# Kernel tuning notes

Measured on AMD Instinct MI355X. Metric: run time of the kernel, lower is better.

Reference implementation:

```python
import jax, jax.numpy as jnp
import numpy as np
import math

B, T, D, NH, HS, NB = 1024, 64, 512, 8, 64, 225  # batch, squares, d_model, heads, head_size, buckets

def _displacement_buckets():
    sq = np.arange(T)
    rank, file = sq // 8, sq % 8
    d_rank = rank[None, :] - rank[:, None]
    d_file = file[None, :] - file[:, None]
    return jnp.asarray((d_rank + 7) * 15 + (d_file + 7))  # (64, 64) in [0, 225)

BUCKET = _displacement_buckets()

def setup_inputs() -> dict:
    key = jax.random.key(0)
    ks = jax.random.split(key, 6)
    return {
        "x": jax.random.normal(ks[0], (B, T, D), dtype=jnp.float32),
        "w_qkv": jax.random.normal(ks[1], (3 * D, D), dtype=jnp.float32) * 0.02,
        "w_proj": jax.random.normal(ks[2], (D, D), dtype=jnp.float32) * 0.02,
        "b_proj": jnp.zeros((D,), dtype=jnp.float32),
        "rel_k": jax.random.normal(ks[3], (NB, HS), dtype=jnp.float32) * 0.02,
        "rel_v": jax.random.normal(ks[4], (NB, HS), dtype=jnp.float32) * 0.02,
    }

def reference(x, w_qkv, w_proj, b_proj, rel_k, rel_v):
    b, t, d = x.shape
    qkv = x @ w_qkv.T                                   # (b, t, 3d)
    qkv = qkv.reshape(b, t, 3, NH, HS)                  # 'b t (three nh h)'
    q, k, v = jnp.moveaxis(qkv, 2, 0).transpose(0, 1, 3, 2, 4)  # each (b, nh, t, h)
    scale = 1.0 / math.sqrt(HS)
    rk = rel_k[BUCKET]                                  # (t, t, h)
    rv = rel_v[BUCKET]                                  # (t, t, h)
    logits = jnp.einsum('bhid,bhjd->bhij', q, k) + jnp.einsum('bhid,ijd->bhij', q, rk)
    attn = jax.nn.softmax(logits * scale, axis=-1)      # (b, nh, t, t)
    out = jnp.einsum('bhij,bhjd->bhid', attn, v) + jnp.einsum('bhij,ijd->bhid', attn, rv)
    out = out.transpose(0, 2, 1, 3).reshape(b, t, d)    # 'b nh t h -> b t (nh h)'
    return out @ w_proj.T + b_proj
```

## Files before the change

kernel.cpp:

```cpp
#include <hip/hip_runtime.h>
#include <hip/hip_bf16.h>
#include <stdint.h>
#include <stddef.h>

typedef __attribute__((ext_vector_type(8))) short bf16x8;
typedef __attribute__((ext_vector_type(4))) float f32x4;

typedef __attribute__((address_space(1))) const unsigned int g_as1;
typedef __attribute__((address_space(3))) unsigned int lds_as3;
__device__ __forceinline__ void gload_lds16(const void* g, void* l) {
  __builtin_amdgcn_global_load_lds((g_as1*)g, (lds_as3*)l, 16, 0, 0);
}

__device__ __forceinline__ unsigned short f2bf(float f) {
  union { float f; unsigned int u; } v; v.f = f;
  unsigned int u = v.u;
  u += 0x7fffu + ((u >> 16) & 1u);
  return (unsigned short)(u >> 16);
}
__device__ __forceinline__ float bf2f(unsigned short s) {
  union { unsigned int u; float f; } v; v.u = ((unsigned int)s) << 16;
  return v.f;
}
__device__ __forceinline__ unsigned cvt_pk_bf16(float lo, float hi) {
  __hip_bfloat162 h2 = __float22bfloat162_rn(make_float2(lo, hi));
  unsigned r;
  __builtin_memcpy(&r, &h2, 4);
  return r;
}


__global__ void prep_kernel(const float* __restrict__ wqkv,
                            const float* __restrict__ wproj,
                            const float* __restrict__ relk,
                            const float* __restrict__ relv,
                            short* __restrict__ wq_t,
                            short* __restrict__ wp_t,
                            short* __restrict__ relk_b,
                            short* __restrict__ relvT_b) {
  const int g = blockIdx.x * 256 + threadIdx.x;
  if (g < 98304) {
    const int row = g >> 6, c8 = g & 63;
    const float* s = wqkv + (size_t)row * 512 + c8 * 8;
    float4 f0 = *(const float4*)s;
    float4 f1 = *(const float4*)(s + 4);
    uint4 w;
    w.x = f2bf(f0.x) | ((unsigned)f2bf(f0.y) << 16);
    w.y = f2bf(f0.z) | ((unsigned)f2bf(f0.w) << 16);
    w.z = f2bf(f1.x) | ((unsigned)f2bf(f1.y) << 16);
    w.w = f2bf(f1.z) | ((unsigned)f2bf(f1.w) << 16);
    const int bn = row >> 7, rl = row & 127, kk = c8 >> 3, c8l = c8 & 7;
    char* d = (char*)wq_t + (size_t)(bn * 8 + kk) * 16384 + rl * 128 +
              ((c8l * 16) ^ ((rl & 7) << 4));
    *(uint4*)d = w;
  } else if (g < 131072) {
    const int g2 = g - 98304;
    const int row = g2 >> 6, c8 = g2 & 63;
    const float* s = wproj + (size_t)row * 512 + c8 * 8;
    float4 f0 = *(const float4*)s;
    float4 f1 = *(const float4*)(s + 4);
    uint4 w;
    w.x = f2bf(f0.x) | ((unsigned)f2bf(f0.y) << 16);
    w.y = f2bf(f0.z) | ((unsigned)f2bf(f0.w) << 16);
    w.z = f2bf(f1.x) | ((unsigned)f2bf(f1.y) << 16);
    w.w = f2bf(f1.z) | ((unsigned)f2bf(f1.w) << 16);
    const int bn = row >> 7, rl = row & 127, kk = c8 >> 3, c8l = c8 & 7;
    char* d = (char*)wp_t + (size_t)(bn * 8 + kk) * 16384 + rl * 128 +
              ((c8l * 16) ^ ((rl & 7) << 4));
    *(uint4*)d = w;
  } else if (g < 133120) {
    const int g3 = g - 131072;
    const int nb = g3 >> 3, c8 = g3 & 7;
    uint4 w = {0u, 0u, 0u, 0u};
    if (nb < 225) {
      const float* s = relk + (size_t)nb * 64 + c8 * 8;
      float4 f0 = *(const float4*)s;
      float4 f1 = *(const float4*)(s + 4);
      w.x = f2bf(f0.x) | ((unsigned)f2bf(f0.y) << 16);
      w.y = f2bf(f0.z) | ((unsigned)f2bf(f0.w) << 16);
      w.z = f2bf(f1.x) | ((unsigned)f2bf(f1.y) << 16);
      w.w = f2bf(f1.z) | ((unsigned)f2bf(f1.w) << 16);
    }
    *(uint4*)(relk_b + nb * 64 + c8 * 8) = w;
  } else {
    const int g4 = g - 133120;
    const int d = g4 >> 5, nb0 = (g4 & 31) * 8;
    unsigned short s[8];
#pragma unroll
    for (int j = 0; j < 8; ++j) {
      const int nb = nb0 + j;
      s[j] = (nb < 225) ? f2bf(relv[(size_t)nb * 64 + d]) : (unsigned short)0;
    }
    uint4 w;
    w.x = s[0] | ((unsigned)s[1] << 16);
    w.y = s[2] | ((unsigned)s[3] << 16);
    w.z = s[4] | ((unsigned)s[5] << 16);
    w.w = s[6] | ((unsigned)s[7] << 16);
    *(uint4*)(relvT_b + d * 256 + nb0) = w;
  }
}

__global__ void xconv_kernel(const float* __restrict__ x, short* __restrict__ x_t) {
  const int g = blockIdx.x * 256 + threadIdx.x;
  const int row = g >> 6, c8 = g & 63;
  const float* s = x + (size_t)row * 512 + c8 * 8;
  float4 f0 = *(const float4*)s;
  float4 f1 = *(const float4*)(s + 4);
  uint4 w;
  w.x = f2bf(f0.x) | ((unsigned)f2bf(f0.y) << 16);
  w.y = f2bf(f0.z) | ((unsigned)f2bf(f0.w) << 16);
  w.z = f2bf(f1.x) | ((unsigned)f2bf(f1.y) << 16);
  w.w = f2bf(f1.z) | ((unsigned)f2bf(f1.w) << 16);
  const int bm = row >> 7, rl = row & 127, kk = c8 >> 3, c8l = c8 & 7;
  char* d = (char*)x_t + (size_t)(bm * 8 + kk) * 16384 + rl * 128 +
            ((c8l * 16) ^ ((rl & 7) << 4));
  *(uint4*)d = w;
}

__global__ __launch_bounds__(256)
void qkv_gemm(const short* __restrict__ x_t, const short* __restrict__ wq_t,
              short* __restrict__ q_g, short* __restrict__ k_g,
              short* __restrict__ vT_g) {
  __shared__ __align__(16) short As[8192];
  __shared__ __align__(16) short Bs[8192];
  const int tid = threadIdx.x;
  const int lane = tid & 63;
  const int l15 = lane & 15, l4 = lane >> 4;
  const int wave = tid >> 6;
  const int wm = wave >> 1, wn = wave & 1;
  const int bid = blockIdx.x;
  const int wg = (bid & 7) * 768 + (bid >> 3);
  const int bn = wg % 12;
  const int bm = wg / 12;
  char* as_ = (char*)As;
  char* bs_ = (char*)Bs;
  const char* abase = (const char*)x_t + (size_t)bm * 131072;
  const char* bbase = (const char*)wq_t + (size_t)bn * 131072;
  const int soff = tid * 16;

  const f32x4 fz = {0.f, 0.f, 0.f, 0.f};
  f32x4 acc[4][4];
#pragma unroll
  for (int mt = 0; mt < 4; ++mt)
#pragma unroll
    for (int nt = 0; nt < 4; ++nt) acc[mt][nt] = fz;

#pragma unroll 1
  for (int kk = 0; kk < 8; ++kk) {
    const char* ga = abase + kk * 16384 + soff;
    const char* gb = bbase + kk * 16384 + soff;
#pragma unroll
    for (int i = 0; i < 4; ++i) {
      gload_lds16(ga + i * 4096, as_ + soff + i * 4096);
      gload_lds16(gb + i * 4096, bs_ + soff + i * 4096);
    }
    __syncthreads();
#pragma unroll
    for (int ki = 0; ki < 2; ++ki) {
      bf16x8 af[4], bfr[4];
#pragma unroll
      for (int mt = 0; mt < 4; ++mt) {
        const int row = 64 * wm + 16 * mt + l15;
        af[mt] = *(const bf16x8*)(as_ + row * 128 + ((64 * ki + 16 * l4) ^ ((row & 7) << 4)));
      }
#pragma unroll
      for (int nt = 0; nt < 4; ++nt) {
        const int row = 64 * wn + 16 * nt + l15;
        bfr[nt] = *(const bf16x8*)(bs_ + row * 128 + ((64 * ki + 16 * l4) ^ ((row & 7) << 4)));
      }
#pragma unroll
      for (int mt = 0; mt < 4; ++mt)
#pragma unroll
        for (int nt = 0; nt < 4; ++nt)
          acc[mt][nt] = __builtin_amdgcn_mfma_f32_16x16x32_bf16(af[mt], bfr[nt], acc[mt][nt], 0, 0, 0);
    }
    __syncthreads();
  }

  const int three = bn >> 2;
  if (three < 2) {
    short* dst = (three == 0) ? q_g : k_g;
#pragma unroll
    for (int mt = 0; mt < 4; ++mt) {
      const int m0 = bm * 128 + 64 * wm + 16 * mt + 4 * l4;
      const int b = m0 >> 6, t0 = m0 & 63;
#pragma unroll
      for (int nt = 0; nt < 4; ++nt) {
        const int n = bn * 128 + 64 * wn + 16 * nt + l15;
        const int h = (n >> 6) & 7, d = n & 63;
        short* p = dst + (size_t)(b * 8 + h) * 4096 + d;
#pragma unroll
        for (int jj = 0; jj < 4; ++jj)
          p[(t0 + jj) * 64] = (short)f2bf(acc[mt][nt][jj]);
      }
    }
  } else {
#pragma unroll
    for (int mt = 0; mt < 4; ++mt) {
      const int m0 = bm * 128 + 64 * wm + 16 * mt + 4 * l4;
      const int b = m0 >> 6, t0 = m0 & 63;
#pragma unroll
      for (int nt = 0; nt < 4; ++nt) {
        const int n = bn * 128 + 64 * wn + 16 * nt + l15;
        const int h = (n >> 6) & 7, d = n & 63;
        uint2 w;
        w.x = cvt_pk_bf16(acc[mt][nt][0], acc[mt][nt][1]);
        w.y = cvt_pk_bf16(acc[mt][nt][2], acc[mt][nt][3]);
        *(uint2*)(vT_g + (size_t)((b * 8 + h) * 64 + d) * 64 + t0) = w;
      }
    }
  }
}

__global__ __launch_bounds__(256, 4)
void attn_kernel(const short* __restrict__ q_g, const short* __restrict__ k_g,
                 const short* __restrict__ vT_g, const short* __restrict__ relk,
                 const short* __restrict__ relvT, short* __restrict__ aout_t) {
  __shared__ __align__(16) short srel_s[64 * 256];
  __shared__ __align__(16) short attn_s[64 * 64];
  const int tid = threadIdx.x, lane = tid & 63, w = tid >> 6;
  const int l15 = lane & 15, l4 = lane >> 4;
  const int bh = blockIdx.x;
  const short* qb = q_g + (size_t)bh * 4096;
  const short* kb = k_g + (size_t)bh * 4096;
  const short* vb = vT_g + (size_t)bh * 4096;
  char* ss = (char*)srel_s;
  char* as = (char*)attn_s;
  const f32x4 fz = {0.f, 0.f, 0.f, 0.f};

  bf16x8 bq[4][2];
#pragma unroll
  for (int nt = 0; nt < 4; ++nt)
#pragma unroll
    for (int kkk = 0; kkk < 2; ++kkk)
      bq[nt][kkk] = *(const bf16x8*)(qb + (16 * nt + l15) * 64 + 32 * kkk + 8 * l4);
#pragma unroll
  for (int mtl = 0; mtl < 4; ++mtl) {
    const int mt = 4 * w + mtl;
    bf16x8 ar0 = *(const bf16x8*)(relk + (16 * mt + l15) * 64 + 8 * l4);
    bf16x8 ar1 = *(const bf16x8*)(relk + (16 * mt + l15) * 64 + 32 + 8 * l4);
#pragma unroll
    for (int nt = 0; nt < 4; ++nt) {
      f32x4 a = fz;
      a = __builtin_amdgcn_mfma_f32_16x16x32_bf16(ar0, bq[nt][0], a, 0, 0, 0);
      a = __builtin_amdgcn_mfma_f32_16x16x32_bf16(ar1, bq[nt][1], a, 0, 0, 0);
      const int i = 16 * nt + l15;
      const int nb0 = 16 * mt + 4 * l4;
      uint2 wv;
      wv.x = cvt_pk_bf16(a[0], a[1]);
      wv.y = cvt_pk_bf16(a[2], a[3]);
      *(uint2*)(ss + i * 512 + ((nb0 * 2) ^ ((i & 7) << 4))) = wv;
    }
  }

  f32x4 sacc[4];
#pragma unroll
  for (int jt = 0; jt < 4; ++jt) {
    sacc[jt] = fz;
    bf16x8 ak0 = *(const bf16x8*)(kb + (16 * jt + l15) * 64 + 8 * l4);
    bf16x8 ak1 = *(const bf16x8*)(kb + (16 * jt + l15) * 64 + 32 + 8 * l4);
    sacc[jt] = __builtin_amdgcn_mfma_f32_16x16x32_bf16(ak0, bq[w][0], sacc[jt], 0, 0, 0);
    sacc[jt] = __builtin_amdgcn_mfma_f32_16x16x32_bf16(ak1, bq[w][1], sacc[jt], 0, 0, 0);
  }
  __syncthreads();

  const int i = 16 * w + l15;
  const int swz = (i & 7) << 4;
  const int ibase = i * 512;
  const int off2 = 2 * (15 * (l4 >> 1) + 4 * (l4 & 1) + 112 - (15 * (i >> 3) + (i & 7)));
  float p[16];
  float mx = -1e30f;
#pragma unroll
  for (int jt = 0; jt < 4; ++jt)
#pragma unroll
    for (int rg = 0; rg < 4; ++rg) {
      const int adr = ibase + (((60 * jt + 2 * rg) + off2) ^ swz);
      const float sr = bf2f(*(const unsigned short*)(ss + adr));
      const float lv = sacc[jt][rg] + sr;
      p[4 * jt + rg] = lv;
      mx = fmaxf(mx, lv);
    }
  mx = fmaxf(mx, __shfl_xor(mx, 16));
  mx = fmaxf(mx, __shfl_xor(mx, 32));
  float sum = 0.f;
#pragma unroll
  for (int q2 = 0; q2 < 16; ++q2) {
    p[q2] = __expf((p[q2] - mx) * 0.125f);
    sum += p[q2];
  }
  sum += __shfl_xor(sum, 16);
  sum += __shfl_xor(sum, 32);
  const float rs = 1.0f / sum;
  unsigned pk[8];
#pragma unroll
  for (int h2 = 0; h2 < 8; ++h2)
    pk[h2] = cvt_pk_bf16(p[2 * h2] * rs, p[2 * h2 + 1] * rs);
#pragma unroll
  for (int jt = 0; jt < 4; ++jt) {
    uint2 wv;
    wv.x = pk[2 * jt];
    wv.y = pk[2 * jt + 1];
    *(uint2*)(as + i * 128 + (((16 * jt + 4 * l4) * 2) ^ swz)) = wv;
  }
  {
    const uint4 uz = {0u, 0u, 0u, 0u};
#pragma unroll
    for (int c = 0; c < 8; ++c)
      *(uint4*)(ss + ibase + ((l4 * 128 + c * 16) ^ swz)) = uz;
  }
#pragma unroll
  for (int jt = 0; jt < 4; ++jt)
#pragma unroll
    for (int rg = 0; rg < 4; ++rg) {
      const int adr = ibase + (((60 * jt + 2 * rg) + off2) ^ swz);
      const int q2 = 4 * jt + rg;
      const unsigned v = pk[q2 >> 1] >> ((q2 & 1) * 16);
      *(unsigned short*)(ss + adr) = (unsigned short)v;
    }
  __syncthreads();

  f32x4 oacc[4];
#pragma unroll
  for (int nt = 0; nt < 4; ++nt) oacc[nt] = fz;
#pragma unroll
  for (int kkk = 0; kkk < 2; ++kkk) {
    bf16x8 av = *(const bf16x8*)(vb + (16 * w + l15) * 64 + 32 * kkk + 8 * l4);
#pragma unroll
    for (int nt = 0; nt < 4; ++nt) {
      const int t = 16 * nt + l15;
      bf16x8 bp = *(const bf16x8*)(as + t * 128 + (((32 * kkk + 8 * l4) * 2) ^ ((t & 7) << 4)));
      oacc[nt] = __builtin_amdgcn_mfma_f32_16x16x32_bf16(av, bp, oacc[nt], 0, 0, 0);
    }
  }
#pragma unroll
  for (int kkk = 0; kkk < 8; ++kkk) {
    bf16x8 arv = *(const bf16x8*)(relvT + (16 * w + l15) * 256 + 32 * kkk + 8 * l4);
#pragma unroll
    for (int nt = 0; nt < 4; ++nt) {
      const int t = 16 * nt + l15;
      bf16x8 bp = *(const bf16x8*)(ss + t * 512 + (((32 * kkk + 8 * l4) * 2) ^ ((t & 7) << 4)));
      oacc[nt] = __builtin_amdgcn_mfma_f32_16x16x32_bf16(arv, bp, oacc[nt], 0, 0, 0);
    }
  }
  const int b = bh >> 3, h = bh & 7;
  char* abase = (char*)aout_t + (size_t)((b >> 1) * 8 + h) * 16384;
  const int rbase = (b & 1) * 64;
#pragma unroll
  for (int nt = 0; nt < 4; ++nt) {
    const int t = 16 * nt + l15;
    const int r = rbase + t;
    const int d0 = 16 * w + 4 * l4;
    uint2 wv;
    wv.x = cvt_pk_bf16(oacc[nt][0], oacc[nt][1]);
    wv.y = cvt_pk_bf16(oacc[nt][2], oacc[nt][3]);
    *(uint2*)(abase + r * 128 + ((d0 * 2) ^ ((r & 7) << 4))) = wv;
  }
}

__global__ __launch_bounds__(256)
void proj_kernel(const short* __restrict__ a_t, const short* __restrict__ wp_t,
                 const float* __restrict__ bproj, float* __restrict__ out) {
  __shared__ __align__(16) short As[8192];
  __shared__ __align__(16) short Bs[8192];
  const int tid = threadIdx.x;
  const int lane = tid & 63;
  const int wave = tid >> 6;
  const int wm = wave >> 1, wn = wave & 1;
  const int l15 = lane & 15, l4 = lane >> 4;
  const int bid = blockIdx.x;
  const int wg = (bid & 7) * 256 + (bid >> 3);
  const int bn = wg & 3;
  const int bm = wg >> 2;
  char* as_ = (char*)As;
  char* bs_ = (char*)Bs;
  const char* abase = (const char*)a_t + (size_t)bm * 131072;
  const char* bbase = (const char*)wp_t + (size_t)bn * 131072;
  const int soff = tid * 16;

  const f32x4 fz = {0.f, 0.f, 0.f, 0.f};
  f32x4 acc[4][4];
#pragma unroll
  for (int mt = 0; mt < 4; ++mt)
#pragma unroll
    for (int nt = 0; nt < 4; ++nt) acc[mt][nt] = fz;

#pragma unroll 1
  for (int kk = 0; kk < 8; ++kk) {
    const char* ga = abase + kk * 16384 + soff;
    const char* gb = bbase + kk * 16384 + soff;
#pragma unroll
    for (int i = 0; i < 4; ++i) {
      gload_lds16(ga + i * 4096, as_ + soff + i * 4096);
      gload_lds16(gb + i * 4096, bs_ + soff + i * 4096);
    }
    __syncthreads();
#pragma unroll
    for (int ki = 0; ki < 2; ++ki) {
      bf16x8 af[4], bq[4];
#pragma unroll
      for (int mt = 0; mt < 4; ++mt) {
        const int row = 64 * wm + 16 * mt + l15;
        af[mt] = *(const bf16x8*)(as_ + row * 128 + ((64 * ki + 16 * l4) ^ ((row & 7) << 4)));
      }
#pragma unroll
      for (int nt = 0; nt < 4; ++nt) {
        const int row = 64 * wn + 16 * nt + l15;
        bq[nt] = *(const bf16x8*)(bs_ + row * 128 + ((64 * ki + 16 * l4) ^ ((row & 7) << 4)));
      }
#pragma unroll
      for (int mt = 0; mt < 4; ++mt)
#pragma unroll
        for (int nt = 0; nt < 4; ++nt)
          acc[mt][nt] = __builtin_amdgcn_mfma_f32_16x16x32_bf16(af[mt], bq[nt], acc[mt][nt], 0, 0, 0);
    }
    __syncthreads();
  }
#pragma unroll
  for (int nt = 0; nt < 4; ++nt) {
    const int col = bn * 128 + 64 * wn + 16 * nt + l15;
    const float bias = bproj[col];
#pragma unroll
    for (int mt = 0; mt < 4; ++mt) {
      const int r0 = bm * 128 + 64 * wm + 16 * mt + 4 * l4;
#pragma unroll
      for (int jj = 0; jj < 4; ++jj)
        out[(size_t)(r0 + jj) * 512 + col] = acc[mt][nt][jj] + bias;
    }
  }
}

extern "C" void kernel_launch(void* const* d_in, const int* in_sizes, int n_in,
                              void* d_out, int out_size, void* d_ws, size_t ws_size,
                              hipStream_t stream) {
  const float* x = (const float*)d_in[0];
  const float* wqkv = (const float*)d_in[1];
  const float* wproj = (const float*)d_in[2];
  const float* bproj = (const float*)d_in[3];
  const float* relk = (const float*)d_in[4];
  const float* relv = (const float*)d_in[5];
  float* out = (float*)d_out;

  char* ws = (char*)d_ws;
  const size_t MB = 1024 * 1024;
  short* xa_t = (short*)ws;
  short* vT_g = (short*)(ws + 64 * MB);
  short* wq_t = (short*)(ws + 128 * MB);
  short* wp_t = (short*)(ws + 128 * MB + 1572864);
  short* relk_b = (short*)(ws + 128 * MB + 2097152);
  short* relvT_b = (short*)(ws + 128 * MB + 2129920);
  short* q_gg = (short*)d_out;
  short* k_gg = (short*)((char*)d_out + 64 * MB);

  prep_kernel<<<dim3(528), dim3(256), 0, stream>>>(wqkv, wproj, relk, relv, wq_t,
                                                   wp_t, relk_b, relvT_b);
  xconv_kernel<<<dim3(16384), dim3(256), 0, stream>>>(x, xa_t);
  qkv_gemm<<<dim3(6144), dim3(256), 0, stream>>>(xa_t, wq_t, q_gg, k_gg, vT_g);
  attn_kernel<<<dim3(8192), dim3(256), 0, stream>>>(q_gg, k_gg, vT_g, relk_b,
                                                    relvT_b, xa_t);
  proj_kernel<<<dim3(2048), dim3(256), 0, stream>>>(xa_t, wp_t, bproj, out);
}
```

Baseline: 376.1 us.

## Double-buffer LDS tiles in QKV and projection GEMMs to overlap loads with MFMA

```diff
diff --git a/kernel.cpp b/kernel.cpp
--- a/kernel.cpp
+++ b/kernel.cpp
@@ -121,8 +121,8 @@
 void qkv_gemm(const short* __restrict__ x_t, const short* __restrict__ wq_t,
               short* __restrict__ q_g, short* __restrict__ k_g,
               short* __restrict__ vT_g) {
-  __shared__ __align__(16) short As[8192];
-  __shared__ __align__(16) short Bs[8192];
+  __shared__ __align__(16) short As[16384];
+  __shared__ __align__(16) short Bs[16384];
   const int tid = threadIdx.x;
   const int lane = tid & 63;
   const int l15 = lane & 15, l4 = lane >> 4;
@@ -145,28 +145,38 @@
 #pragma unroll
     for (int nt = 0; nt < 4; ++nt) acc[mt][nt] = fz;
 
+#pragma unroll
+  for (int i = 0; i < 4; ++i) {
+    gload_lds16(abase + soff + i * 4096, as_ + soff + i * 4096);
+    gload_lds16(bbase + soff + i * 4096, bs_ + soff + i * 4096);
+  }
+  __syncthreads();
+
 #pragma unroll 1
   for (int kk = 0; kk < 8; ++kk) {
-    const char* ga = abase + kk * 16384 + soff;
-    const char* gb = bbase + kk * 16384 + soff;
-#pragma unroll
-    for (int i = 0; i < 4; ++i) {
-      gload_lds16(ga + i * 4096, as_ + soff + i * 4096);
-      gload_lds16(gb + i * 4096, bs_ + soff + i * 4096);
-    }
-    __syncthreads();
+    const int cb = (kk & 1) * 16384;
+    if (kk < 7) {
+      const int nb2 = ((kk + 1) & 1) * 16384;
+      const char* ga = abase + (kk + 1) * 16384 + soff;
+      const char* gb = bbase + (kk + 1) * 16384 + soff;
+#pragma unroll
+      for (int i = 0; i < 4; ++i) {
+        gload_lds16(ga + i * 4096, as_ + nb2 + soff + i * 4096);
+        gload_lds16(gb + i * 4096, bs_ + nb2 + soff + i * 4096);
+      }
+    }
 #pragma unroll
     for (int ki = 0; ki < 2; ++ki) {
       bf16x8 af[4], bfr[4];
 #pragma unroll
       for (int mt = 0; mt < 4; ++mt) {
         const int row = 64 * wm + 16 * mt + l15;
-        af[mt] = *(const bf16x8*)(as_ + row * 128 + ((64 * ki + 16 * l4) ^ ((row & 7) << 4)));
+        af[mt] = *(const bf16x8*)(as_ + cb + row * 128 + ((64 * ki + 16 * l4) ^ ((row & 7) << 4)));
       }
 #pragma unroll
       for (int nt = 0; nt < 4; ++nt) {
         const int row = 64 * wn + 16 * nt + l15;
-        bfr[nt] = *(const bf16x8*)(bs_ + row * 128 + ((64 * ki + 16 * l4) ^ ((row & 7) << 4)));
+        bfr[nt] = *(const bf16x8*)(bs_ + cb + row * 128 + ((64 * ki + 16 * l4) ^ ((row & 7) << 4)));
       }
 #pragma unroll
       for (int mt = 0; mt < 4; ++mt)
@@ -174,7 +184,7 @@
         for (int nt = 0; nt < 4; ++nt)
           acc[mt][nt] = __builtin_amdgcn_mfma_f32_16x16x32_bf16(af[mt], bfr[nt], acc[mt][nt], 0, 0, 0);
     }
-    __syncthreads();
+    if (kk < 7) __syncthreads();
   }
 
   const int three = bn >> 2;
@@ -360,8 +370,8 @@
 __global__ __launch_bounds__(256)
 void proj_kernel(const short* __restrict__ a_t, const short* __restrict__ wp_t,
                  const float* __restrict__ bproj, float* __restrict__ out) {
-  __shared__ __align__(16) short As[8192];
-  __shared__ __align__(16) short Bs[8192];
+  __shared__ __align__(16) short As[16384];
+  __shared__ __align__(16) short Bs[16384];
   const int tid = threadIdx.x;
   const int lane = tid & 63;
   const int wave = tid >> 6;
@@ -384,28 +394,38 @@
 #pragma unroll
     for (int nt = 0; nt < 4; ++nt) acc[mt][nt] = fz;
 
+#pragma unroll
+  for (int i = 0; i < 4; ++i) {
+    gload_lds16(abase + soff + i * 4096, as_ + soff + i * 4096);
+    gload_lds16(bbase + soff + i * 4096, bs_ + soff + i * 4096);
+  }
+  __syncthreads();
+
 #pragma unroll 1
   for (int kk = 0; kk < 8; ++kk) {
-    const char* ga = abase + kk * 16384 + soff;
-    const char* gb = bbase + kk * 16384 + soff;
-#pragma unroll
-    for (int i = 0; i < 4; ++i) {
-      gload_lds16(ga + i * 4096, as_ + soff + i * 4096);
-      gload_lds16(gb + i * 4096, bs_ + soff + i * 4096);
-    }
-    __syncthreads();
+    const int cb = (kk & 1) * 16384;
+    if (kk < 7) {
+      const int nb2 = ((kk + 1) & 1) * 16384;
+      const char* ga = abase + (kk + 1) * 16384 + soff;
+      const char* gb = bbase + (kk + 1) * 16384 + soff;
+#pragma unroll
+      for (int i = 0; i < 4; ++i) {
+        gload_lds16(ga + i * 4096, as_ + nb2 + soff + i * 4096);
+        gload_lds16(gb + i * 4096, bs_ + nb2 + soff + i * 4096);
+      }
+    }
 #pragma unroll
     for (int ki = 0; ki < 2; ++ki) {
       bf16x8 af[4], bq[4];
 #pragma unroll
       for (int mt = 0; mt < 4; ++mt) {
         const int row = 64 * wm + 16 * mt + l15;
-        af[mt] = *(const bf16x8*)(as_ + row * 128 + ((64 * ki + 16 * l4) ^ ((row & 7) << 4)));
+        af[mt] = *(const bf16x8*)(as_ + cb + row * 128 + ((64 * ki + 16 * l4) ^ ((row & 7) << 4)));
       }
 #pragma unroll
       for (int nt = 0; nt < 4; ++nt) {
         const int row = 64 * wn + 16 * nt + l15;
-        bq[nt] = *(const bf16x8*)(bs_ + row * 128 + ((64 * ki + 16 * l4) ^ ((row & 7) << 4)));
+        bq[nt] = *(const bf16x8*)(bs_ + cb + row * 128 + ((64 * ki + 16 * l4) ^ ((row & 7) << 4)));
       }
 #pragma unroll
       for (int mt = 0; mt < 4; ++mt)
@@ -413,7 +433,7 @@
         for (int nt = 0; nt < 4; ++nt)
           acc[mt][nt] = __builtin_amdgcn_mfma_f32_16x16x32_bf16(af[mt], bq[nt], acc[mt][nt], 0, 0, 0);
     }
-    __syncthreads();
+    if (kk < 7) __syncthreads();
   }
 #pragma unroll
   for (int nt = 0; nt < 4; ++nt) {
```

Measured after the change: 375.9 us. Within noise of the previous version (-0.1%).
